# Performance work log

Hardware: AMD Instinct MI355X
Metric: run time of the kernel (lower is better)

The kernel has to match this reference:

```python
import jax, jax.numpy as jnp
import numpy as np
from math import sqrt

D_MODEL = 1024
N_HEADS = 16
FF_MULT = 4
MAX_DIST = 512
LN_EPS = 1e-5


def layer_norm(x, g, b):
    mu = jnp.mean(x, axis=-1, keepdims=True)
    var = jnp.var(x, axis=-1, keepdims=True)
    return (x - mu) * jax.lax.rsqrt(var + LN_EPS) * g + b


def setup_inputs() -> dict:
    key = jax.random.key(0)
    ks = jax.random.split(key, 10)
    D, H, F = D_MODEL, N_HEADS, D_MODEL * FF_MULT
    s = 0.02
    return {
        "x": jax.random.normal(ks[0], (2, 2048, D), dtype=jnp.float32),
        "w_qkv": jax.random.normal(ks[1], (D, 3 * D), dtype=jnp.float32) * s,
        "b_qkv": jnp.zeros((3 * D,), jnp.float32),
        "w_out": jax.random.normal(ks[2], (D, D), dtype=jnp.float32) * s,
        "b_out": jnp.zeros((D,), jnp.float32),
        "rel_bias": jax.random.normal(ks[3], (2 * MAX_DIST + 1, H), dtype=jnp.float32) * s,
        "g1": jnp.ones((D,), jnp.float32),
        "beta1": jnp.zeros((D,), jnp.float32),
        "w1": jax.random.normal(ks[4], (D, F), dtype=jnp.float32) * s,
        "b1": jnp.zeros((F,), jnp.float32),
        "w2": jax.random.normal(ks[5], (F, D), dtype=jnp.float32) * s,
        "b2": jnp.zeros((D,), jnp.float32),
        "g2": jnp.ones((D,), jnp.float32),
        "beta2": jnp.zeros((D,), jnp.float32),
    }


def reference(x, w_qkv, b_qkv, w_out, b_out, rel_bias, g1, beta1, w1, b1, w2, b2, g2, beta2):
    B, T, D = x.shape
    H = N_HEADS
    hd = D // H
    qkv = x @ w_qkv + b_qkv                      # [B,T,3D]
    q, k, v = jnp.split(qkv, 3, axis=-1)
    # [B,H,T,hd]
    q = q.reshape(B, T, H, hd).transpose(0, 2, 1, 3)
    k = k.reshape(B, T, H, hd).transpose(0, 2, 1, 3)
    v = v.reshape(B, T, H, hd).transpose(0, 2, 1, 3)
    scores = jnp.einsum("bhqd,bhkd->bhqk", q, k) / sqrt(hd)
    # relative position bias: gather from table [2*max_dist+1, H]
    rel = jnp.clip(jnp.arange(T)[None, :] - jnp.arange(T)[:, None], -MAX_DIST, MAX_DIST) + MAX_DIST
    bias = rel_bias[rel].transpose(2, 0, 1)       # [H,T,T]
    attn = jax.nn.softmax(scores + bias[None], axis=-1)
    out = jnp.einsum("bhqk,bhkd->bhqd", attn, v).transpose(0, 2, 1, 3).reshape(B, T, D)
    out = out @ w_out + b_out                     # dropout inactive (eval)
    x2 = layer_norm(x + out, g1, beta1)
    ff = jax.nn.gelu(x2 @ w1 + b1, approximate=False) @ w2 + b2
    x3 = layer_norm(x2 + ff, g2, beta2)
    return (x3, attn)
```

## Files before the change

kernel.cpp:

```cpp
#include <hip/hip_runtime.h>
#include <hip/hip_bf16.h>
#include <cstdint>
#include <cstddef>

#define DEVFN static __device__ __forceinline__

typedef __attribute__((ext_vector_type(8))) short bf16x8;
typedef __attribute__((ext_vector_type(4))) float f32x4;

#define WAITVM(N) asm volatile("s_waitcnt vmcnt(" #N ")" ::: "memory")
#define WAITLGKM() asm volatile("s_waitcnt lgkmcnt(0)" ::: "memory")
#define BAR() __builtin_amdgcn_s_barrier()

DEVFN float exp2f_fast(float x) { return __builtin_amdgcn_exp2f(x); }

DEVFN ushort f2bf(float f) {
  uint32_t u = __float_as_uint(f);
  return (ushort)((u + 0x7fffu + ((u >> 16) & 1u)) >> 16);
}
DEVFN float bf2f(ushort u) { return __uint_as_float((uint32_t)u << 16); }

DEVFN void gl_lds16(const void* g, void* l) {
  __builtin_amdgcn_global_load_lds(
      (const __attribute__((address_space(1))) void*)g,
      (__attribute__((address_space(3))) void*)l, 16, 0, 0);
}

DEVFN float wred_sum(float v) {
#pragma unroll
  for (int o = 32; o; o >>= 1) v += __shfl_xor(v, o);
  return v;
}


__global__ __launch_bounds__(256) void pack_bf16(const float* __restrict__ in,
                                                 ushort* __restrict__ out) {
  size_t i = ((size_t)blockIdx.x * 256 + threadIdx.x) * 4;
  float4 v = *(const float4*)&in[i];
  ushort4 u = make_ushort4(f2bf(v.x), f2bf(v.y), f2bf(v.z), f2bf(v.w));
  *(ushort4*)&out[i] = u;
}

__global__ __launch_bounds__(256) void wtrans(const float* __restrict__ in,
                                              ushort* __restrict__ out,
                                              int K, int N) {
  __shared__ float tile[32][33];
  int n0 = blockIdx.x * 32, k0 = blockIdx.y * 32;
  int tid = threadIdx.x;
#pragma unroll
  for (int i = 0; i < 4; ++i) {
    int idx = tid + i * 256;
    int r = idx >> 5, c = idx & 31;
    tile[r][c] = in[(size_t)(k0 + r) * N + n0 + c];
  }
  __syncthreads();
#pragma unroll
  for (int i = 0; i < 4; ++i) {
    int idx = tid + i * 256;
    int r = idx >> 5, c = idx & 31;
    out[(size_t)(n0 + r) * K + k0 + c] = f2bf(tile[c][r]);
  }
}

__global__ __launch_bounds__(256) void pack_vT(const ushort* __restrict__ qkv,
                                               ushort* __restrict__ vT) {
  __shared__ ushort tile[64][72];
  int bh = blockIdx.y, b = bh >> 4, h = bh & 15;
  int t0 = blockIdx.x * 64;
  int tid = threadIdx.x;
#pragma unroll
  for (int i = 0; i < 16; ++i) {
    int idx = tid + i * 256;
    int r = idx >> 6, c = idx & 63;
    tile[r][c] = qkv[(size_t)(b * 2048 + t0 + r) * 3072 + 2048 + h * 64 + c];
  }
  __syncthreads();
#pragma unroll
  for (int i = 0; i < 16; ++i) {
    int idx = tid + i * 256;
    int d = idx >> 6, t = idx & 63;
    vT[((size_t)bh * 64 + d) * 2048 + t0 + t] = tile[t][d];
  }
}


template <bool GELU, bool STF32, bool STBF16>
__global__ __launch_bounds__(256)
void gemm128(const ushort* __restrict__ A, int lda,
             const ushort* __restrict__ BT, int ldb,
             const float* __restrict__ bias,
             float* __restrict__ Cf, ushort* __restrict__ Cb, int ldc, int K) {
  __shared__ ushort lsa[128 * 64];
  __shared__ ushort lsb[128 * 64];
  const int tid = threadIdx.x;
  const int lane = tid & 63;
  const int wv = tid >> 6;
  const int wr = (wv >> 1) * 64, wc = (wv & 1) * 64;
  const ushort* Ab = A + (size_t)blockIdx.y * 128 * lda;
  const ushort* Bb = BT + (size_t)blockIdx.x * 128 * ldb;
  f32x4 acc[4][4] = {};
  int rowS[4], slotS[4];
#pragma unroll
  for (int i = 0; i < 4; ++i) {
    int idx = tid + i * 256;
    rowS[i] = idx >> 3;
    slotS[i] = (idx & 7) ^ (rowS[i] & 7);
  }
  for (int kt = 0; kt < K; kt += 64) {
    __syncthreads();
#pragma unroll
    for (int i = 0; i < 4; ++i) {
      gl_lds16(Ab + (size_t)rowS[i] * lda + kt + slotS[i] * 8, &lsa[(tid + i * 256) * 8]);
      gl_lds16(Bb + (size_t)rowS[i] * ldb + kt + slotS[i] * 8, &lsb[(tid + i * 256) * 8]);
    }
    asm volatile("s_waitcnt vmcnt(0)" ::: "memory");
    __syncthreads();
#pragma unroll
    for (int kk = 0; kk < 2; ++kk) {
      bf16x8 af[4], bfr[4];
      const int g = kk * 4 + (lane >> 4);
#pragma unroll
      for (int m = 0; m < 4; ++m) {
        int r = wr + m * 16 + (lane & 15);
        af[m] = *(const bf16x8*)&lsa[r * 64 + ((g ^ (r & 7)) * 8)];
      }
#pragma unroll
      for (int n = 0; n < 4; ++n) {
        int r = wc + n * 16 + (lane & 15);
        bfr[n] = *(const bf16x8*)&lsb[r * 64 + ((g ^ (r & 7)) * 8)];
      }
#pragma unroll
      for (int m = 0; m < 4; ++m)
#pragma unroll
        for (int n = 0; n < 4; ++n)
          acc[m][n] = __builtin_amdgcn_mfma_f32_16x16x32_bf16(af[m], bfr[n], acc[m][n], 0, 0, 0);
    }
  }
  const int rb = blockIdx.y * 128 + wr + ((lane >> 4) << 2);
  const int cb = blockIdx.x * 128 + wc + (lane & 15);
#pragma unroll
  for (int m = 0; m < 4; ++m)
#pragma unroll
    for (int n = 0; n < 4; ++n) {
      int col = cb + n * 16;
      float bv = bias[col];
#pragma unroll
      for (int i = 0; i < 4; ++i) {
        int row = rb + m * 16 + i;
        float v = acc[m][n][i] + bv;
        if (GELU) v = 0.5f * v * (1.0f + erff(v * 0.70710678f));
        if (STF32) Cf[(size_t)row * ldc + col] = v;
        if (STBF16) Cb[(size_t)row * ldc + col] = f2bf(v);
      }
    }
}


__global__ __launch_bounds__(256, 2)
void attn_fused(const ushort* __restrict__ qkv, const ushort* __restrict__ vT,
                const float* __restrict__ rel_bias,
                float* __restrict__ attn, ushort* __restrict__ ctx) {
  __shared__ ushort lsq[128 * 64];
  __shared__ ushort lsk[2][64 * 64];
  __shared__ ushort lsv[2][64 * 64];
  __shared__ ushort lsp[128 * 64];
  __shared__ float biasl[1025];
  const int tid = threadIdx.x;
  const int lane = tid & 63;
  const int wv = tid >> 6;
  const int bh = blockIdx.y, b = bh >> 4, h = bh & 15;
  const int q0 = blockIdx.x * 128;
  const ushort* qp = qkv + (size_t)b * 2048 * 3072 + h * 64;
  const ushort* kp = qp + 1024;
  const ushort* vp = vT + (size_t)bh * 64 * 2048;
  float* attnb = attn + (size_t)bh * 2048 * 2048;
  const float C_SC = 0.18033688011f;

  for (int i = tid; i < 1025; i += 256) biasl[i] = rel_bias[i * 16 + h] * 1.44269504f;

#pragma unroll
  for (int i = 0; i < 4; ++i) {
    int idx = tid + i * 256;
    int row = idx >> 3;
    int slot = (idx & 7) ^ (row & 7);
    gl_lds16(qp + (size_t)(q0 + row) * 3072 + slot * 8, &lsq[idx * 8]);
  }

  const int r0 = tid >> 3;
  const int sl0 = (tid & 7) ^ (r0 & 7);
  const int r1 = (tid + 256) >> 3;
  const int sl1 = ((tid + 256) & 7) ^ (r1 & 7);

  auto stageK = [&](int t, int buf) {
    gl_lds16(kp + (size_t)(t * 64 + r0) * 3072 + sl0 * 8, &lsk[buf][tid * 8]);
    gl_lds16(kp + (size_t)(t * 64 + r1) * 3072 + sl1 * 8, &lsk[buf][(tid + 256) * 8]);
  };
  auto stageV = [&](int t, int buf) {
    gl_lds16(vp + (size_t)r0 * 2048 + t * 64 + sl0 * 8, &lsv[buf][tid * 8]);
    gl_lds16(vp + (size_t)r1 * 2048 + t * 64 + sl1 * 8, &lsv[buf][(tid + 256) * 8]);
  };

  auto mfmaS = [&](int buf, f32x4 accs[2][4]) {
    __builtin_amdgcn_s_setprio(1);
#pragma unroll
    for (int kk = 0; kk < 2; ++kk) {
      const int g = kk * 4 + (lane >> 4);
      bf16x8 aq[2], bk[4];
#pragma unroll
      for (int m = 0; m < 2; ++m) {
        int r = wv * 32 + m * 16 + (lane & 15);
        aq[m] = *(const bf16x8*)&lsq[r * 64 + ((g ^ (r & 7)) * 8)];
      }
#pragma unroll
      for (int n = 0; n < 4; ++n) {
        int r = n * 16 + (lane & 15);
        bk[n] = *(const bf16x8*)&lsk[buf][r * 64 + ((g ^ (r & 7)) * 8)];
      }
#pragma unroll
      for (int m = 0; m < 2; ++m)
#pragma unroll
        for (int n = 0; n < 4; ++n)
          accs[m][n] = __builtin_amdgcn_mfma_f32_16x16x32_bf16(aq[m], bk[n], accs[m][n], 0, 0, 0);
    }
    __builtin_amdgcn_s_setprio(0);
  };

  WAITLGKM();

  float l_part[8];
#pragma unroll
  for (int j = 0; j < 8; ++j) l_part[j] = 0.0f;

  stageK(0, 0);
  for (int t = 0; t < 32; ++t) {
    if (t < 31) {
      stageK(t + 1, (t + 1) & 1);
      WAITVM(2);
    } else {
      WAITVM(0);
    }
    BAR();
    f32x4 accs[2][4] = {};
    mfmaS(t & 1, accs);
#pragma unroll
    for (int m = 0; m < 2; ++m)
#pragma unroll
      for (int n = 0; n < 4; ++n)
#pragma unroll
        for (int i = 0; i < 4; ++i) {
          int row = q0 + wv * 32 + m * 16 + ((lane >> 4) << 2) + i;
          int col = t * 64 + n * 16 + (lane & 15);
          int rel = col - row;
          rel = rel < -512 ? -512 : (rel > 512 ? 512 : rel);
          l_part[m * 4 + i] += exp2f_fast(fmaf(accs[m][n][i], C_SC, biasl[rel + 512]));
        }
    BAR();
  }

  float inv_l[8];
#pragma unroll
  for (int j = 0; j < 8; ++j) {
    float l = l_part[j];
    l += __shfl_xor(l, 1);
    l += __shfl_xor(l, 2);
    l += __shfl_xor(l, 4);
    l += __shfl_xor(l, 8);
    inv_l[j] = 1.0f / l;
  }

  f32x4 acc_o[2][4] = {};
  stageK(0, 0);
  stageV(0, 0);
  for (int t = 0; t < 32; ++t) {
    if (t < 31) {
      stageK(t + 1, (t + 1) & 1);
      stageV(t + 1, (t + 1) & 1);
    }
    if (t == 0) { WAITVM(4); }
    else if (t < 31) { WAITVM(36); }
    else { WAITVM(32); }
    BAR();
    f32x4 accs[2][4] = {};
    mfmaS(t & 1, accs);
#pragma unroll
    for (int m = 0; m < 2; ++m)
#pragma unroll
      for (int n = 0; n < 4; ++n)
#pragma unroll
        for (int i = 0; i < 4; ++i) {
          int rloc = wv * 32 + m * 16 + ((lane >> 4) << 2) + i;
          int col = n * 16 + (lane & 15);
          int rel = (t * 64 + col) - (q0 + rloc);
          rel = rel < -512 ? -512 : (rel > 512 ? 512 : rel);
          float p = exp2f_fast(fmaf(accs[m][n][i], C_SC, biasl[rel + 512])) * inv_l[m * 4 + i];
          lsp[rloc * 64 + (((col >> 3) ^ (rloc & 7)) << 3) + (col & 7)] = f2bf(p);
          attnb[(size_t)(q0 + rloc) * 2048 + t * 64 + col] = p;
        }
    WAITLGKM();
    BAR();
    __builtin_amdgcn_s_setprio(1);
#pragma unroll
    for (int kk = 0; kk < 2; ++kk) {
      const int g = kk * 4 + (lane >> 4);
      bf16x8 ap[2], bv2[4];
#pragma unroll
      for (int m = 0; m < 2; ++m) {
        int r = wv * 32 + m * 16 + (lane & 15);
        ap[m] = *(const bf16x8*)&lsp[r * 64 + ((g ^ (r & 7)) * 8)];
      }
#pragma unroll
      for (int n = 0; n < 4; ++n) {
        int r = n * 16 + (lane & 15);
        bv2[n] = *(const bf16x8*)&lsv[t & 1][r * 64 + ((g ^ (r & 7)) * 8)];
      }
#pragma unroll
      for (int m = 0; m < 2; ++m)
#pragma unroll
        for (int n = 0; n < 4; ++n)
          acc_o[m][n] = __builtin_amdgcn_mfma_f32_16x16x32_bf16(ap[m], bv2[n], acc_o[m][n], 0, 0, 0);
    }
    __builtin_amdgcn_s_setprio(0);
  }

#pragma unroll
  for (int m = 0; m < 2; ++m)
#pragma unroll
    for (int n = 0; n < 4; ++n) {
      int col = h * 64 + n * 16 + (lane & 15);
#pragma unroll
      for (int i = 0; i < 4; ++i) {
        int row = q0 + wv * 32 + m * 16 + ((lane >> 4) << 2) + i;
        ctx[(size_t)(b * 2048 + row) * 1024 + col] = f2bf(acc_o[m][n][i]);
      }
    }
}


__global__ __launch_bounds__(256)
void add_ln(const float* __restrict__ a, const float* __restrict__ r,
            const float* __restrict__ g, const float* __restrict__ be,
            float* __restrict__ outf, ushort* __restrict__ outb) {
  const int tid = threadIdx.x;
  const size_t base = (size_t)blockIdx.x * 1024 + tid * 4;
  float4 va = *(const float4*)&a[base];
  float4 vr = *(const float4*)&r[base];
  float x0 = va.x + vr.x, x1 = va.y + vr.y, x2 = va.z + vr.z, x3 = va.w + vr.w;
  float s = x0 + x1 + x2 + x3;
  float s2 = x0 * x0 + x1 * x1 + x2 * x2 + x3 * x3;
  s = wred_sum(s);
  s2 = wred_sum(s2);
  __shared__ float rs[4], rq[4];
  if ((tid & 63) == 0) { rs[tid >> 6] = s; rq[tid >> 6] = s2; }
  __syncthreads();
  s = rs[0] + rs[1] + rs[2] + rs[3];
  s2 = rq[0] + rq[1] + rq[2] + rq[3];
  const float mean = s * (1.0f / 1024.0f);
  const float var = s2 * (1.0f / 1024.0f) - mean * mean;
  const float sc = rsqrtf(var + 1e-5f);
  float4 vg = *(const float4*)&g[tid * 4];
  float4 vb = *(const float4*)&be[tid * 4];
  float y0 = (x0 - mean) * sc * vg.x + vb.x;
  float y1 = (x1 - mean) * sc * vg.y + vb.y;
  float y2 = (x2 - mean) * sc * vg.z + vb.z;
  float y3 = (x3 - mean) * sc * vg.w + vb.w;
  *(float4*)&outf[base] = make_float4(y0, y1, y2, y3);
  if (outb) {
    ushort4 u = make_ushort4(f2bf(y0), f2bf(y1), f2bf(y2), f2bf(y3));
    *(ushort4*)&outb[base] = u;
  }
}


extern "C" void kernel_launch(void* const* d_in, const int* in_sizes, int n_in,
                              void* d_out, int out_size, void* d_ws, size_t ws_size,
                              hipStream_t stream) {
  const float* x     = (const float*)d_in[0];
  const float* w_qkv = (const float*)d_in[1];
  const float* b_qkv = (const float*)d_in[2];
  const float* w_out = (const float*)d_in[3];
  const float* b_out = (const float*)d_in[4];
  const float* relb  = (const float*)d_in[5];
  const float* g1    = (const float*)d_in[6];
  const float* be1   = (const float*)d_in[7];
  const float* w1    = (const float*)d_in[8];
  const float* b1    = (const float*)d_in[9];
  const float* w2    = (const float*)d_in[10];
  const float* b2    = (const float*)d_in[11];
  const float* g2    = (const float*)d_in[12];
  const float* be2   = (const float*)d_in[13];

  float* x3o  = (float*)d_out;
  float* attn = x3o + (size_t)4194304;

  char* w = (char*)d_ws;
  size_t off = 0;
  auto alloc = [&](size_t bytes) {
    void* p = w + off;
    off += (bytes + 255) & ~(size_t)255;
    return p;
  };
  ushort* x_bf   = (ushort*)alloc(4096ull * 1024 * 2);
  ushort* wqkvT  = (ushort*)alloc(3072ull * 1024 * 2);
  ushort* woutT  = (ushort*)alloc(1024ull * 1024 * 2);
  ushort* w1T    = (ushort*)alloc(4096ull * 1024 * 2);
  ushort* w2T    = (ushort*)alloc(1024ull * 4096 * 2);
  ushort* qkv_bf = (ushort*)alloc(4096ull * 3072 * 2);
  ushort* vT     = (ushort*)alloc(32ull * 64 * 2048 * 2);
  ushort* ctx_bf = (ushort*)alloc(4096ull * 1024 * 2);
  float*  projf  = (float*)alloc(4096ull * 1024 * 4);
  float*  x2f    = (float*)alloc(4096ull * 1024 * 4);
  ushort* x2bf   = (ushort*)alloc(4096ull * 1024 * 2);
  ushort* ff1_bf = (ushort*)alloc(4096ull * 4096 * 2);
  float*  ff2f   = projf;

  pack_bf16<<<4096, 256, 0, stream>>>(x, x_bf);
  wtrans<<<dim3(96, 32), 256, 0, stream>>>(w_qkv, wqkvT, 1024, 3072);
  wtrans<<<dim3(32, 32), 256, 0, stream>>>(w_out, woutT, 1024, 1024);
  wtrans<<<dim3(128, 32), 256, 0, stream>>>(w1, w1T, 1024, 4096);
  wtrans<<<dim3(32, 128), 256, 0, stream>>>(w2, w2T, 4096, 1024);

  gemm128<false, false, true><<<dim3(24, 32), 256, 0, stream>>>(
      x_bf, 1024, wqkvT, 1024, b_qkv, nullptr, qkv_bf, 3072, 1024);
  pack_vT<<<dim3(32, 32), 256, 0, stream>>>(qkv_bf, vT);
  attn_fused<<<dim3(16, 32), 256, 0, stream>>>(qkv_bf, vT, relb, attn, ctx_bf);

  gemm128<false, true, false><<<dim3(8, 32), 256, 0, stream>>>(
      ctx_bf, 1024, woutT, 1024, b_out, projf, nullptr, 1024, 1024);
  add_ln<<<4096, 256, 0, stream>>>(x, projf, g1, be1, x2f, x2bf);
  gemm128<true, false, true><<<dim3(32, 32), 256, 0, stream>>>(
      x2bf, 1024, w1T, 1024, b1, nullptr, ff1_bf, 4096, 1024);
  gemm128<false, true, false><<<dim3(8, 32), 256, 0, stream>>>(
      ff1_bf, 4096, w2T, 4096, b2, ff2f, nullptr, 1024, 4096);
  add_ln<<<4096, 256, 0, stream>>>(x2f, ff2f, g2, be2, x3o, nullptr);
}
```

Before: 513.9 us.

## Transpose QK^T MFMA in attention so each lane owns four contiguous key columns

Computes S^T = K·Q^T with Q fragments held in registers, so each lane holds four consecutive key positions for a single query row. This lets the attention probability writes go out as float4 stores and the LDS P writes as ushort4, instead of scattered scalar stores. The relative-bias table gets padding so four adjacent bias values can be read from one clamped base index. Tiles that are fully outside the clip range use a single constant bias. The trade-off is more live registers for the Q fragments and more complex index logic.

Measured after the change: 502.4 us. 2.2% less time.

```diff
diff --git a/kernel.cpp b/kernel.cpp
--- a/kernel.cpp
+++ b/kernel.cpp
@@ -18,7 +18,6 @@
   uint32_t u = __float_as_uint(f);
   return (ushort)((u + 0x7fffu + ((u >> 16) & 1u)) >> 16);
 }
-DEVFN float bf2f(ushort u) { return __uint_as_float((uint32_t)u << 16); }
 
 DEVFN void gl_lds16(const void* g, void* l) {
   __builtin_amdgcn_global_load_lds(
@@ -164,10 +163,12 @@
   __shared__ ushort lsk[2][64 * 64];
   __shared__ ushort lsv[2][64 * 64];
   __shared__ ushort lsp[128 * 64];
-  __shared__ float biasl[1025];
+  __shared__ float extb[1034];
   const int tid = threadIdx.x;
   const int lane = tid & 63;
   const int wv = tid >> 6;
+  const int hi = lane >> 4;
+  const int lo = lane & 15;
   const int bh = blockIdx.y, b = bh >> 4, h = bh & 15;
   const int q0 = blockIdx.x * 128;
   const ushort* qp = qkv + (size_t)b * 2048 * 3072 + h * 64;
@@ -176,7 +177,11 @@
   float* attnb = attn + (size_t)bh * 2048 * 2048;
   const float C_SC = 0.18033688011f;
 
-  for (int i = tid; i < 1025; i += 256) biasl[i] = rel_bias[i * 16 + h] * 1.44269504f;
+  for (int i = tid; i < 1034; i += 256) {
+    int j = i - 3;
+    j = j < 0 ? 0 : (j > 1024 ? 1024 : j);
+    extb[i] = rel_bias[j * 16 + h] * 1.44269504f;
+  }
 
 #pragma unroll
   for (int i = 0; i < 4; ++i) {
@@ -185,6 +190,19 @@
     int slot = (idx & 7) ^ (row & 7);
     gl_lds16(qp + (size_t)(q0 + row) * 3072 + slot * 8, &lsq[idx * 8]);
   }
+  WAITVM(0);
+  WAITLGKM();
+  BAR();
+
+  bf16x8 qf[2][2];
+#pragma unroll
+  for (int mq = 0; mq < 2; ++mq)
+#pragma unroll
+    for (int kk = 0; kk < 2; ++kk) {
+      int r = wv * 32 + mq * 16 + lo;
+      int g = kk * 4 + hi;
+      qf[mq][kk] = *(const bf16x8*)&lsq[r * 64 + ((g ^ (r & 7)) * 8)];
+    }
 
   const int r0 = tid >> 3;
   const int sl0 = (tid & 7) ^ (r0 & 7);
@@ -200,37 +218,28 @@
     gl_lds16(vp + (size_t)r1 * 2048 + t * 64 + sl1 * 8, &lsv[buf][(tid + 256) * 8]);
   };
 
-  auto mfmaS = [&](int buf, f32x4 accs[2][4]) {
+  auto mfmaS = [&](int buf, f32x4 sacc[4][2]) {
     __builtin_amdgcn_s_setprio(1);
 #pragma unroll
     for (int kk = 0; kk < 2; ++kk) {
-      const int g = kk * 4 + (lane >> 4);
-      bf16x8 aq[2], bk[4];
-#pragma unroll
-      for (int m = 0; m < 2; ++m) {
-        int r = wv * 32 + m * 16 + (lane & 15);
-        aq[m] = *(const bf16x8*)&lsq[r * 64 + ((g ^ (r & 7)) * 8)];
-      }
-#pragma unroll
-      for (int n = 0; n < 4; ++n) {
-        int r = n * 16 + (lane & 15);
-        bk[n] = *(const bf16x8*)&lsk[buf][r * 64 + ((g ^ (r & 7)) * 8)];
-      }
-#pragma unroll
-      for (int m = 0; m < 2; ++m)
-#pragma unroll
-        for (int n = 0; n < 4; ++n)
-          accs[m][n] = __builtin_amdgcn_mfma_f32_16x16x32_bf16(aq[m], bk[n], accs[m][n], 0, 0, 0);
+      const int g = kk * 4 + hi;
+      bf16x8 ak[4];
+#pragma unroll
+      for (int mk = 0; mk < 4; ++mk) {
+        int r = mk * 16 + lo;
+        ak[mk] = *(const bf16x8*)&lsk[buf][r * 64 + ((g ^ (r & 7)) * 8)];
+      }
+#pragma unroll
+      for (int mk = 0; mk < 4; ++mk)
+#pragma unroll
+        for (int mq = 0; mq < 2; ++mq)
+          sacc[mk][mq] =
+              __builtin_amdgcn_mfma_f32_16x16x32_bf16(ak[mk], qf[mq][kk], sacc[mk][mq], 0, 0, 0);
     }
     __builtin_amdgcn_s_setprio(0);
   };
 
-  WAITLGKM();
-
-  float l_part[8];
-#pragma unroll
-  for (int j = 0; j < 8; ++j) l_part[j] = 0.0f;
-
+  float l_part[2] = {0.0f, 0.0f};
   stageK(0, 0);
   for (int t = 0; t < 32; ++t) {
     if (t < 31) {
@@ -240,32 +249,49 @@
       WAITVM(0);
     }
     BAR();
-    f32x4 accs[2][4] = {};
-    mfmaS(t & 1, accs);
-#pragma unroll
-    for (int m = 0; m < 2; ++m)
-#pragma unroll
-      for (int n = 0; n < 4; ++n)
-#pragma unroll
-        for (int i = 0; i < 4; ++i) {
-          int row = q0 + wv * 32 + m * 16 + ((lane >> 4) << 2) + i;
-          int col = t * 64 + n * 16 + (lane & 15);
-          int rel = col - row;
-          rel = rel < -512 ? -512 : (rel > 512 ? 512 : rel);
-          l_part[m * 4 + i] += exp2f_fast(fmaf(accs[m][n][i], C_SC, biasl[rel + 512]));
+    f32x4 sacc[4][2] = {};
+    mfmaS(t & 1, sacc);
+    const bool farR = (t * 64) >= q0 + 640;
+    const bool farL = (t * 64 + 63) <= q0 - 512;
+    if (farR || farL) {
+      const float bc = farR ? extb[3 + 1024] : extb[3];
+#pragma unroll
+      for (int mq = 0; mq < 2; ++mq) {
+        float s = 0.0f;
+#pragma unroll
+        for (int mk = 0; mk < 4; ++mk)
+#pragma unroll
+          for (int i = 0; i < 4; ++i)
+            s += exp2f_fast(fmaf(sacc[mk][mq][i], C_SC, bc));
+        l_part[mq] += s;
+      }
+    } else {
+      const int kbase = t * 64 + hi * 4;
+      const int qr = q0 + wv * 32 + lo;
+#pragma unroll
+      for (int mq = 0; mq < 2; ++mq) {
+        float s = 0.0f;
+#pragma unroll
+        for (int mk = 0; mk < 4; ++mk) {
+          int k0 = (kbase + mk * 16) - (qr + mq * 16) + 515;
+          k0 = k0 < 0 ? 0 : (k0 > 1030 ? 1030 : k0);
+#pragma unroll
+          for (int i = 0; i < 4; ++i)
+            s += exp2f_fast(fmaf(sacc[mk][mq][i], C_SC, extb[k0 + i]));
         }
+        l_part[mq] += s;
+      }
+    }
     BAR();
   }
 
-  float inv_l[8];
-#pragma unroll
-  for (int j = 0; j < 8; ++j) {
-    float l = l_part[j];
-    l += __shfl_xor(l, 1);
-    l += __shfl_xor(l, 2);
-    l += __shfl_xor(l, 4);
-    l += __shfl_xor(l, 8);
-    inv_l[j] = 1.0f / l;
+  float inv_l[2];
+#pragma unroll
+  for (int mq = 0; mq < 2; ++mq) {
+    float l = l_part[mq];
+    l += __shfl_xor(l, 16);
+    l += __shfl_xor(l, 32);
+    inv_l[mq] = 1.0f / l;
   }
 
   f32x4 acc_o[2][4] = {};
@@ -277,40 +303,53 @@
       stageV(t + 1, (t + 1) & 1);
     }
     if (t == 0) { WAITVM(4); }
-    else if (t < 31) { WAITVM(36); }
-    else { WAITVM(32); }
+    else if (t < 31) { WAITVM(12); }
+    else { WAITVM(8); }
     BAR();
-    f32x4 accs[2][4] = {};
-    mfmaS(t & 1, accs);
-#pragma unroll
-    for (int m = 0; m < 2; ++m)
-#pragma unroll
-      for (int n = 0; n < 4; ++n)
-#pragma unroll
-        for (int i = 0; i < 4; ++i) {
-          int rloc = wv * 32 + m * 16 + ((lane >> 4) << 2) + i;
-          int col = n * 16 + (lane & 15);
-          int rel = (t * 64 + col) - (q0 + rloc);
-          rel = rel < -512 ? -512 : (rel > 512 ? 512 : rel);
-          float p = exp2f_fast(fmaf(accs[m][n][i], C_SC, biasl[rel + 512])) * inv_l[m * 4 + i];
-          lsp[rloc * 64 + (((col >> 3) ^ (rloc & 7)) << 3) + (col & 7)] = f2bf(p);
-          attnb[(size_t)(q0 + rloc) * 2048 + t * 64 + col] = p;
+    f32x4 sacc[4][2] = {};
+    mfmaS(t & 1, sacc);
+    const bool farT = ((t * 64) >= q0 + 640) || ((t * 64 + 63) <= q0 - 512);
+    const float bcf = ((t * 64) >= q0 + 640) ? extb[3 + 1024] : extb[3];
+#pragma unroll
+    for (int mq = 0; mq < 2; ++mq) {
+      const int row = wv * 32 + mq * 16 + lo;
+      const float il = inv_l[mq];
+#pragma unroll
+      for (int mk = 0; mk < 4; ++mk) {
+        const int c0 = mk * 16 + hi * 4;
+        float p4[4];
+        if (farT) {
+#pragma unroll
+          for (int i = 0; i < 4; ++i)
+            p4[i] = exp2f_fast(fmaf(sacc[mk][mq][i], C_SC, bcf)) * il;
+        } else {
+          int k0 = (t * 64 + c0) - (q0 + row) + 515;
+          k0 = k0 < 0 ? 0 : (k0 > 1030 ? 1030 : k0);
+#pragma unroll
+          for (int i = 0; i < 4; ++i)
+            p4[i] = exp2f_fast(fmaf(sacc[mk][mq][i], C_SC, extb[k0 + i])) * il;
         }
+        ushort4 u = make_ushort4(f2bf(p4[0]), f2bf(p4[1]), f2bf(p4[2]), f2bf(p4[3]));
+        *(ushort4*)&lsp[row * 64 + (((c0 >> 3) ^ (row & 7)) << 3) + (c0 & 7)] = u;
+        *(float4*)&attnb[(size_t)(q0 + row) * 2048 + t * 64 + c0] =
+            make_float4(p4[0], p4[1], p4[2], p4[3]);
+      }
+    }
     WAITLGKM();
     BAR();
     __builtin_amdgcn_s_setprio(1);
 #pragma unroll
     for (int kk = 0; kk < 2; ++kk) {
-      const int g = kk * 4 + (lane >> 4);
+      const int g = kk * 4 + hi;
       bf16x8 ap[2], bv2[4];
 #pragma unroll
       for (int m = 0; m < 2; ++m) {
-        int r = wv * 32 + m * 16 + (lane & 15);
+        int r = wv * 32 + m * 16 + lo;
         ap[m] = *(const bf16x8*)&lsp[r * 64 + ((g ^ (r & 7)) * 8)];
       }
 #pragma unroll
       for (int n = 0; n < 4; ++n) {
-        int r = n * 16 + (lane & 15);
+        int r = n * 16 + lo;
         bv2[n] = *(const bf16x8*)&lsv[t & 1][r * 64 + ((g ^ (r & 7)) * 8)];
       }
 #pragma unroll
@@ -326,10 +365,10 @@
   for (int m = 0; m < 2; ++m)
 #pragma unroll
     for (int n = 0; n < 4; ++n) {
-      int col = h * 64 + n * 16 + (lane & 15);
+      int col = h * 64 + n * 16 + lo;
 #pragma unroll
       for (int i = 0; i < 4; ++i) {
-        int row = q0 + wv * 32 + m * 16 + ((lane >> 4) << 2) + i;
+        int row = q0 + wv * 32 + m * 16 + (hi << 2) + i;
         ctx[(size_t)(b * 2048 + row) * 1024 + col] = f2bf(acc_o[m][n][i]);
       }
     }
```
